# Kernel tuning notes

Measured on AMD Instinct MI355X. Metric: run time of the kernel, lower is better.

The kernel has to match this reference:

```python
import jax, jax.numpy as jnp
import numpy as np

N, E, IN = 100000, 1600000, 128
H, C = 4, 16            # heads, out_channels
HID = H * C             # concat output dim = 64
SLOPE = 0.2             # GATv2Conv negative_slope default
EPS = 1e-5              # LayerNorm eps


def setup_inputs() -> dict:
    key = jax.random.key(0)
    ks = jax.random.split(key, 12)
    s = 0.05
    x = jax.random.normal(ks[0], (N, IN), jnp.float32)
    edge_index = jax.random.randint(ks[1], (2, E), 0, N, dtype=jnp.int32)
    return {
        "x": x,
        "edge_index": edge_index,
        # GATv2Conv params (lin_l: source, lin_r: target; both with bias)
        "W_l": jax.random.normal(ks[2], (IN, HID), jnp.float32) * s,
        "b_l": jnp.zeros((HID,), jnp.float32),
        "W_r": jax.random.normal(ks[3], (IN, HID), jnp.float32) * s,
        "b_r": jnp.zeros((HID,), jnp.float32),
        "att": jax.random.normal(ks[4], (H, C), jnp.float32) * s,
        "bias": jnp.zeros((HID,), jnp.float32),
        # residual projection Linear(in, heads*out, bias=False)
        "W_res": jax.random.normal(ks[5], (IN, HID), jnp.float32) * s,
        # pyg LayerNorm affine params
        "ln_w": jnp.ones((HID,), jnp.float32),
        "ln_b": jnp.zeros((HID,), jnp.float32),
    }


def reference(x, edge_index, W_l, b_l, W_r, b_r, att, bias, W_res, ln_w, ln_b):
    n = x.shape[0]
    # GATv2Conv adds self-loops by default
    loops = jnp.arange(n, dtype=edge_index.dtype)
    src = jnp.concatenate([edge_index[0], loops])  # message source j
    dst = jnp.concatenate([edge_index[1], loops])  # message target i

    xl = (x @ W_l + b_l).reshape(n, H, C)  # source-side projection
    xr = (x @ W_r + b_r).reshape(n, H, C)  # target-side projection

    # GATv2 attention: e_ij = att . LeakyReLU(xl_j + xr_i)
    e = jax.nn.leaky_relu(xl[src] + xr[dst], SLOPE)   # [Et, H, C]
    score = jnp.einsum('ehc,hc->eh', e, att)          # [Et, H]

    # segment softmax over incoming edges of each target node
    smax = jax.ops.segment_max(score, dst, num_segments=n)
    ex = jnp.exp(score - smax[dst])
    ssum = jax.ops.segment_sum(ex, dst, num_segments=n)
    alpha = ex / (ssum[dst] + 1e-16)                  # [Et, H]

    # weighted scatter-add of source features, concat heads
    msg = xl[src] * alpha[..., None]                  # [Et, H, C]
    out = jax.ops.segment_sum(msg, dst, num_segments=n).reshape(n, HID)
    out = out + bias + x @ W_res                      # bias + residual

    # pyg.nn.LayerNorm(mode='graph', batch=None): global mean/std over all elems
    out = out - out.mean()
    out = out / (out.std() + EPS)
    return out * ln_w + ln_b
```

## Files before the change

### kernel.cpp

```cpp
#include <hip/hip_runtime.h>
#include <math.h>

#define SLOPE  0.2f
#define LN_EPS 1e-5f
#define HID    64
#define IN_DIM 128
#define BM     64

__global__ __launch_bounds__(256) void proj_kernel(
    const float* __restrict__ x,
    const float* __restrict__ Wl, const float* __restrict__ bl,
    const float* __restrict__ Wr, const float* __restrict__ br,
    const float* __restrict__ Wres,
    float* __restrict__ xl, float* __restrict__ xr, float* __restrict__ out_un,
    int n)
{
    __shared__ float xs[BM][132];
    int t = threadIdx.x;
    int row0 = blockIdx.x * BM;

#pragma unroll
    for (int p = 0; p < 8; ++p) {
        int f  = t + p * 256;
        int r  = f >> 5;
        int c4 = f & 31;
        float4 v = make_float4(0.f, 0.f, 0.f, 0.f);
        if (row0 + r < n) v = ((const float4*)x)[(long)(row0 + r) * 32 + c4];
        *(float4*)&xs[r][c4 * 4] = v;
    }
    __syncthreads();

    int cb = (t & 15) * 4;
    int ry = (t >> 4) * 4;

    float4 acc[3][4];
#pragma unroll
    for (int r = 0; r < 4; ++r) {
        acc[0][r] = *(const float4*)&bl[cb];
        acc[1][r] = *(const float4*)&br[cb];
        acc[2][r] = make_float4(0.f, 0.f, 0.f, 0.f);
    }

    for (int k4 = 0; k4 < 32; ++k4) {
        float4 xv[4];
#pragma unroll
        for (int r = 0; r < 4; ++r)
            xv[r] = *(const float4*)&xs[ry + r][k4 * 4];
#pragma unroll
        for (int kk = 0; kk < 4; ++kk) {
            int k = k4 * 4 + kk;
            float4 w0 = *(const float4*)&Wl  [k * HID + cb];
            float4 w1 = *(const float4*)&Wr  [k * HID + cb];
            float4 w2 = *(const float4*)&Wres[k * HID + cb];
#pragma unroll
            for (int r = 0; r < 4; ++r) {
                float xvk = (kk == 0) ? xv[r].x : (kk == 1) ? xv[r].y
                          : (kk == 2) ? xv[r].z : xv[r].w;
                acc[0][r].x = fmaf(xvk, w0.x, acc[0][r].x);
                acc[0][r].y = fmaf(xvk, w0.y, acc[0][r].y);
                acc[0][r].z = fmaf(xvk, w0.z, acc[0][r].z);
                acc[0][r].w = fmaf(xvk, w0.w, acc[0][r].w);
                acc[1][r].x = fmaf(xvk, w1.x, acc[1][r].x);
                acc[1][r].y = fmaf(xvk, w1.y, acc[1][r].y);
                acc[1][r].z = fmaf(xvk, w1.z, acc[1][r].z);
                acc[1][r].w = fmaf(xvk, w1.w, acc[1][r].w);
                acc[2][r].x = fmaf(xvk, w2.x, acc[2][r].x);
                acc[2][r].y = fmaf(xvk, w2.y, acc[2][r].y);
                acc[2][r].z = fmaf(xvk, w2.z, acc[2][r].z);
                acc[2][r].w = fmaf(xvk, w2.w, acc[2][r].w);
            }
        }
    }

#pragma unroll
    for (int r = 0; r < 4; ++r) {
        long ro = row0 + ry + r;
        if (ro < n) {
            *(float4*)&xl    [ro * HID + cb] = acc[0][r];
            *(float4*)&xr    [ro * HID + cb] = acc[1][r];
            *(float4*)&out_un[ro * HID + cb] = acc[2][r];
        }
    }
}

__global__ void deg_zero_kernel(int* __restrict__ deg, int n) {
    for (int i = blockIdx.x * blockDim.x + threadIdx.x; i < n; i += gridDim.x * blockDim.x)
        deg[i] = 0;
}

__global__ __launch_bounds__(256) void rank_kernel(
    const int* __restrict__ dst, int* __restrict__ deg, int* __restrict__ rank, int e)
{
    int tid = blockIdx.x * blockDim.x + threadIdx.x;
    int stride = gridDim.x * blockDim.x;
    int e4 = e >> 2;
    for (int i = tid; i < e4; i += stride) {
        int4 d = ((const int4*)dst)[i];
        int r0 = atomicAdd(&deg[d.x], 1);
        int r1 = atomicAdd(&deg[d.y], 1);
        int r2 = atomicAdd(&deg[d.z], 1);
        int r3 = atomicAdd(&deg[d.w], 1);
        ((int4*)rank)[i] = make_int4(r0, r1, r2, r3);
    }
    for (int i = (e4 << 2) + tid; i < e; i += stride)
        rank[i] = atomicAdd(&deg[dst[i]], 1);
}

__global__ __launch_bounds__(1024) void scan_kernel(
    const int* __restrict__ deg, int* __restrict__ off, int n)
{
    __shared__ int wsum[16];
    __shared__ int carry_s;
    int t = threadIdx.x, lane = t & 63, w = t >> 6;
    if (t == 0) carry_s = 0;
    __syncthreads();
    for (int base = 0; base < n; base += 4096) {
        int i0 = base + t * 4;
        int4 v = make_int4(0, 0, 0, 0);
        if (i0 + 3 < n) {
            int4 dv = *(const int4*)&deg[i0];
            v = make_int4(dv.x + 1, dv.y + 1, dv.z + 1, dv.w + 1);
        } else if (i0 < n) {
            v.x = deg[i0] + 1;
            if (i0 + 1 < n) v.y = deg[i0 + 1] + 1;
            if (i0 + 2 < n) v.z = deg[i0 + 2] + 1;
        }
        int local = v.x + v.y + v.z + v.w;
        int inc = local;
#pragma unroll
        for (int d = 1; d < 64; d <<= 1) {
            int o = __shfl_up(inc, d, 64);
            if (lane >= d) inc += o;
        }
        if (lane == 63) wsum[w] = inc;
        __syncthreads();
        if (w == 0 && lane < 16) {
            int s = wsum[lane];
#pragma unroll
            for (int d = 1; d < 16; d <<= 1) {
                int o = __shfl_up(s, d, 16);
                if (lane >= d) s += o;
            }
            wsum[lane] = s;
        }
        __syncthreads();
        int woff = (w > 0) ? wsum[w - 1] : 0;
        int bc = carry_s;
        __syncthreads();
        int o0 = bc + woff + inc - local;
        int o1 = o0 + v.x, o2 = o1 + v.y, o3 = o2 + v.z;
        if (i0     < n) off[i0]     = o0;
        if (i0 + 1 < n) off[i0 + 1] = o1;
        if (i0 + 2 < n) off[i0 + 2] = o2;
        if (i0 + 3 < n) off[i0 + 3] = o3;
        if (t == 1023) carry_s = bc + wsum[15];
        __syncthreads();
    }
    if (threadIdx.x == 0) off[n] = carry_s;
}

__global__ __launch_bounds__(256) void place_kernel(
    const int* __restrict__ src, const int* __restrict__ dst,
    const int* __restrict__ rank, const int* __restrict__ off,
    int* __restrict__ csr, int e)
{
    int tid = blockIdx.x * blockDim.x + threadIdx.x;
    int stride = gridDim.x * blockDim.x;
    int e4 = e >> 2;
    for (int i = tid; i < e4; i += stride) {
        int4 d = ((const int4*)dst)[i];
        int4 s = ((const int4*)src)[i];
        int4 r = ((const int4*)rank)[i];
        int o0 = off[d.x], o1 = off[d.y], o2 = off[d.z], o3 = off[d.w];
        csr[o0 + r.x] = s.x;
        csr[o1 + r.y] = s.y;
        csr[o2 + r.z] = s.z;
        csr[o3 + r.w] = s.w;
    }
    for (int i = (e4 << 2) + tid; i < e; i += stride)
        csr[off[dst[i]] + rank[i]] = src[i];
}

__global__ void selfloop_kernel(const int* __restrict__ off, const int* __restrict__ deg,
                                int* __restrict__ csr, int n)
{
    for (int i = blockIdx.x * blockDim.x + threadIdx.x; i < n; i += gridDim.x * blockDim.x)
        csr[off[i] + deg[i]] = i;
}

__global__ __launch_bounds__(256) void attn_kernel(
    const float* __restrict__ xl, const float* __restrict__ xr,
    const float* __restrict__ att, const float* __restrict__ bias,
    const int* __restrict__ off, const int* __restrict__ csr,
    float* __restrict__ out_un,
    float2* __restrict__ partials, int n)
{
    int lane = threadIdx.x & 63;
    int wid  = threadIdx.x >> 6;
    int node = blockIdx.x * 4 + wid;

    float s1 = 0.0f, s2 = 0.0f;
    if (node < n) {
        float a    = att[lane];
        float bi   = bias[lane];
        float xr_v = xr[(long)node * HID + lane];

        int e0 = off[node], e1 = off[node + 1];

        float m = -INFINITY, ssum = 0.0f, acc = 0.0f;

#define ATT_UPDATE(vv)                                                    \
        {                                                                 \
            float tt = (vv) + xr_v;                                       \
            tt = (tt > 0.0f) ? tt : SLOPE * tt;                           \
            float pp = tt * a;                                            \
            pp += __shfl_xor(pp, 1, 16);                                  \
            pp += __shfl_xor(pp, 2, 16);                                  \
            pp += __shfl_xor(pp, 4, 16);                                  \
            pp += __shfl_xor(pp, 8, 16);                                  \
            float nm = fmaxf(m, pp);                                      \
            float eo = __expf(m - nm);                                    \
            float pe = __expf(pp - nm);                                   \
            acc  = acc * eo + pe * (vv);                                  \
            ssum = ssum * eo + pe;                                        \
            m = nm;                                                       \
        }

        int e = e0;
        for (; e + 4 <= e1; e += 4) {
            int j0 = csr[e], j1 = csr[e + 1], j2 = csr[e + 2], j3 = csr[e + 3];
            float v0 = xl[(long)j0 * HID + lane];
            float v1 = xl[(long)j1 * HID + lane];
            float v2 = xl[(long)j2 * HID + lane];
            float v3 = xl[(long)j3 * HID + lane];
            ATT_UPDATE(v0); ATT_UPDATE(v1); ATT_UPDATE(v2); ATT_UPDATE(v3);
        }
        for (; e < e1; ++e) {
            int j = csr[e];
            float v = xl[(long)j * HID + lane];
            ATT_UPDATE(v);
        }
#undef ATT_UPDATE

        float r = acc / (ssum + 1e-16f) + bi + out_un[(long)node * HID + lane];
        out_un[(long)node * HID + lane] = r;
        s1 = r; s2 = r * r;
    }

#pragma unroll
    for (int d = 32; d; d >>= 1) {
        s1 += __shfl_xor(s1, d, 64);
        s2 += __shfl_xor(s2, d, 64);
    }
    __shared__ float bs[8];
    if (lane == 0) { bs[wid] = s1; bs[4 + wid] = s2; }
    __syncthreads();
    if (threadIdx.x == 0)
        partials[blockIdx.x] = make_float2(bs[0] + bs[1] + bs[2] + bs[3],
                                           bs[4] + bs[5] + bs[6] + bs[7]);
}

__global__ __launch_bounds__(1024) void reduce_kernel(
    const float2* __restrict__ partials, double* __restrict__ red, int nb)
{
    double a = 0.0, b = 0.0;
    for (int i = threadIdx.x; i < nb; i += 1024) {
        float2 p = partials[i];
        a += (double)p.x; b += (double)p.y;
    }
#pragma unroll
    for (int d = 32; d; d >>= 1) {
        a += __shfl_xor(a, d, 64);
        b += __shfl_xor(b, d, 64);
    }
    __shared__ double sa[16], sb[16];
    int w = threadIdx.x >> 6;
    if ((threadIdx.x & 63) == 0) { sa[w] = a; sb[w] = b; }
    __syncthreads();
    if (threadIdx.x == 0) {
        double ta = 0.0, tb = 0.0;
#pragma unroll
        for (int k = 0; k < 16; ++k) { ta += sa[k]; tb += sb[k]; }
        red[0] = ta; red[1] = tb;
    }
}

__global__ void ln_kernel(const float* __restrict__ out_un, const double* __restrict__ red,
                          const float* __restrict__ ln_w, const float* __restrict__ ln_b,
                          float* __restrict__ out, int total )
{
    double cnt  = (double)total;
    double mu   = red[0] / cnt;
    double var  = red[1] / cnt - mu * mu;
    float mean  = (float)mu;
    float inv   = 1.0f / (sqrtf((float)(var > 0.0 ? var : 0.0)) + LN_EPS);
    int n4 = total >> 2;
    for (int i = blockIdx.x * blockDim.x + threadIdx.x; i < n4; i += gridDim.x * blockDim.x) {
        float4 v = ((const float4*)out_un)[i];
        int cb = (i << 2) & 63;
        float4 r;
        r.x = (v.x - mean) * inv * ln_w[cb + 0] + ln_b[cb + 0];
        r.y = (v.y - mean) * inv * ln_w[cb + 1] + ln_b[cb + 1];
        r.z = (v.z - mean) * inv * ln_w[cb + 2] + ln_b[cb + 2];
        r.w = (v.w - mean) * inv * ln_w[cb + 3] + ln_b[cb + 3];
        ((float4*)out)[i] = r;
    }
}

extern "C" void kernel_launch(void* const* d_in, const int* in_sizes, int n_in,
                              void* d_out, int out_size, void* d_ws, size_t ws_size,
                              hipStream_t stream)
{
    const float* x    = (const float*)d_in[0];
    const int*   ei   = (const int*)d_in[1];
    const float* Wl   = (const float*)d_in[2];
    const float* bl   = (const float*)d_in[3];
    const float* Wr   = (const float*)d_in[4];
    const float* br   = (const float*)d_in[5];
    const float* att  = (const float*)d_in[6];
    const float* bias = (const float*)d_in[7];
    const float* Wres = (const float*)d_in[8];
    const float* lnw  = (const float*)d_in[9];
    const float* lnb  = (const float*)d_in[10];

    int n = in_sizes[0] / IN_DIM;
    int e = in_sizes[1] / 2;
    const int* src = ei;
    const int* dst = ei + e;

    int nblocks = (n + 3) / 4;

    char* w = (char*)d_ws;
    double* red    = (double*)w;
    float* xl      = (float*)(w + 256);
    float* xr      = xl + (long)n * HID;
    float* out_un  = xr + (long)n * HID;
    int*   deg     = (int*)(out_un + (long)n * HID);
    int*   off     = deg + n;
    int*   csr     = off + n + 1;
    int*    rank     = (int*)out_un;
    float2* partials = (float2*)deg;

    deg_zero_kernel<<<512, 256, 0, stream>>>(deg, n);
    rank_kernel<<<1024, 256, 0, stream>>>(dst, deg, rank, e);
    scan_kernel<<<1, 1024, 0, stream>>>(deg, off, n);
    place_kernel<<<1024, 256, 0, stream>>>(src, dst, rank, off, csr, e);
    selfloop_kernel<<<512, 256, 0, stream>>>(off, deg, csr, n);

    proj_kernel<<<(n + BM - 1) / BM, 256, 0, stream>>>(x, Wl, bl, Wr, br, Wres,
                                                       xl, xr, out_un, n);

    attn_kernel<<<nblocks, 256, 0, stream>>>(xl, xr, att, bias, off, csr,
                                             out_un, partials, n);
    reduce_kernel<<<1, 1024, 0, stream>>>(partials, red, nblocks);

    ln_kernel<<<4096, 256, 0, stream>>>(out_un, red, lnw, lnb, (float*)d_out, n * HID);
}
```

Before: 462.8 us.

## Process four edges per wavefront with float4 lanes and fold self-loops into scan

The attention kernel now splits each wavefront into four 16-lane groups. Each group handles a different edge using float4 loads, so four edges are processed per iteration, and the online-softmax states are merged across groups at the end with shuffles. This is meant to raise memory-level parallelism in the gather and cut the shuffle reductions per edge. The self-loop kernel is removed, with the scan writing self-loop entries directly, and the rank and place grids are doubled. The cost is extra exp and merge work plus masked lanes on low-degree nodes.

```diff
diff --git a/kernel.cpp b/kernel.cpp
--- a/kernel.cpp
+++ b/kernel.cpp
@@ -107,7 +107,7 @@
 }
 
 __global__ __launch_bounds__(1024) void scan_kernel(
-    const int* __restrict__ deg, int* __restrict__ off, int n)
+    const int* __restrict__ deg, int* __restrict__ off, int* __restrict__ csr, int n)
 {
     __shared__ int wsum[16];
     __shared__ int carry_s;
@@ -148,11 +148,11 @@
         int bc = carry_s;
         __syncthreads();
         int o0 = bc + woff + inc - local;
-        int o1 = o0 + v.x, o2 = o1 + v.y, o3 = o2 + v.z;
-        if (i0     < n) off[i0]     = o0;
-        if (i0 + 1 < n) off[i0 + 1] = o1;
-        if (i0 + 2 < n) off[i0 + 2] = o2;
-        if (i0 + 3 < n) off[i0 + 3] = o3;
+        int o1 = o0 + v.x, o2 = o1 + v.y, o3 = o2 + v.z, o4 = o3 + v.w;
+        if (i0     < n) { off[i0]     = o0; csr[o1 - 1] = i0;     }
+        if (i0 + 1 < n) { off[i0 + 1] = o1; csr[o2 - 1] = i0 + 1; }
+        if (i0 + 2 < n) { off[i0 + 2] = o2; csr[o3 - 1] = i0 + 2; }
+        if (i0 + 3 < n) { off[i0 + 3] = o3; csr[o4 - 1] = i0 + 3; }
         if (t == 1023) carry_s = bc + wsum[15];
         __syncthreads();
     }
@@ -181,13 +181,6 @@
         csr[off[dst[i]] + rank[i]] = src[i];
 }
 
-__global__ void selfloop_kernel(const int* __restrict__ off, const int* __restrict__ deg,
-                                int* __restrict__ csr, int n)
-{
-    for (int i = blockIdx.x * blockDim.x + threadIdx.x; i < n; i += gridDim.x * blockDim.x)
-        csr[off[i] + deg[i]] = i;
-}
-
 __global__ __launch_bounds__(256) void attn_kernel(
     const float* __restrict__ xl, const float* __restrict__ xr,
     const float* __restrict__ att, const float* __restrict__ bias,
@@ -195,56 +188,79 @@
     float* __restrict__ out_un,
     float2* __restrict__ partials, int n)
 {
-    int lane = threadIdx.x & 63;
-    int wid  = threadIdx.x >> 6;
-    int node = blockIdx.x * 4 + wid;
+    const int l    = threadIdx.x & 63;
+    const int wid  = threadIdx.x >> 6;
+    const int g    = l >> 4;
+    const int r    = l & 15;
+    const int node = blockIdx.x * 4 + wid;
 
     float s1 = 0.0f, s2 = 0.0f;
     if (node < n) {
-        float a    = att[lane];
-        float bi   = bias[lane];
-        float xr_v = xr[(long)node * HID + lane];
+        const float4 a4  = ((const float4*)att)[r];
+        const float4 xr4 = ((const float4*)xr)[node * 16 + r];
 
         int e0 = off[node], e1 = off[node + 1];
-
-        float m = -INFINITY, ssum = 0.0f, acc = 0.0f;
-
-#define ATT_UPDATE(vv)                                                    \
-        {                                                                 \
-            float tt = (vv) + xr_v;                                       \
-            tt = (tt > 0.0f) ? tt : SLOPE * tt;                           \
-            float pp = tt * a;                                            \
-            pp += __shfl_xor(pp, 1, 16);                                  \
-            pp += __shfl_xor(pp, 2, 16);                                  \
-            pp += __shfl_xor(pp, 4, 16);                                  \
-            pp += __shfl_xor(pp, 8, 16);                                  \
-            float nm = fmaxf(m, pp);                                      \
-            float eo = __expf(m - nm);                                    \
-            float pe = __expf(pp - nm);                                   \
-            acc  = acc * eo + pe * (vv);                                  \
-            ssum = ssum * eo + pe;                                        \
-            m = nm;                                                       \
-        }
-
-        int e = e0;
-        for (; e + 4 <= e1; e += 4) {
-            int j0 = csr[e], j1 = csr[e + 1], j2 = csr[e + 2], j3 = csr[e + 3];
-            float v0 = xl[(long)j0 * HID + lane];
-            float v1 = xl[(long)j1 * HID + lane];
-            float v2 = xl[(long)j2 * HID + lane];
-            float v3 = xl[(long)j3 * HID + lane];
-            ATT_UPDATE(v0); ATT_UPDATE(v1); ATT_UPDATE(v2); ATT_UPDATE(v3);
-        }
-        for (; e < e1; ++e) {
-            int j = csr[e];
-            float v = xl[(long)j * HID + lane];
-            ATT_UPDATE(v);
-        }
-#undef ATT_UPDATE
-
-        float r = acc / (ssum + 1e-16f) + bi + out_un[(long)node * HID + lane];
-        out_un[(long)node * HID + lane] = r;
-        s1 = r; s2 = r * r;
+        int nit = (e1 - e0 + 3) >> 2;
+
+        float m = -1e30f, ssum = 0.0f;
+        float4 acc = make_float4(0.f, 0.f, 0.f, 0.f);
+
+        for (int it = 0; it < nit; ++it) {
+            int eidx = e0 + it * 4 + g;
+            bool valid = eidx < e1;
+            int j = csr[valid ? eidx : e1 - 1];
+            float4 v = ((const float4*)xl)[j * 16 + r];
+            float tx = v.x + xr4.x, ty = v.y + xr4.y;
+            float tz = v.z + xr4.z, tw = v.w + xr4.w;
+            tx = fmaxf(tx, SLOPE * tx); ty = fmaxf(ty, SLOPE * ty);
+            tz = fmaxf(tz, SLOPE * tz); tw = fmaxf(tw, SLOPE * tw);
+            float p = fmaf(tw, a4.w, fmaf(tz, a4.z, fmaf(ty, a4.y, tx * a4.x)));
+            p += __shfl_xor(p, 1);
+            p += __shfl_xor(p, 2);
+            float s  = valid ? p : -INFINITY;
+            float nm = fmaxf(m, s);
+            float eo = __expf(m - nm);
+            float pe = __expf(s - nm);
+            acc.x = acc.x * eo + pe * v.x;
+            acc.y = acc.y * eo + pe * v.y;
+            acc.z = acc.z * eo + pe * v.z;
+            acc.w = acc.w * eo + pe * v.w;
+            ssum  = ssum * eo + pe;
+            m = nm;
+        }
+
+#pragma unroll
+        for (int mask = 16; mask <= 32; mask <<= 1) {
+            float om = __shfl_xor(m, mask);
+            float os = __shfl_xor(ssum, mask);
+            float ox = __shfl_xor(acc.x, mask);
+            float oy = __shfl_xor(acc.y, mask);
+            float oz = __shfl_xor(acc.z, mask);
+            float ow = __shfl_xor(acc.w, mask);
+            float nm = fmaxf(m, om);
+            float f1 = __expf(m - nm);
+            float f2 = __expf(om - nm);
+            acc.x = acc.x * f1 + ox * f2;
+            acc.y = acc.y * f1 + oy * f2;
+            acc.z = acc.z * f1 + oz * f2;
+            acc.w = acc.w * f1 + ow * f2;
+            ssum  = ssum * f1 + os * f2;
+            m = nm;
+        }
+
+        float inv = 1.0f / (ssum + 1e-16f);
+        if (l < 16) {
+            float4 b4  = ((const float4*)bias)[r];
+            float4 res = ((const float4*)out_un)[node * 16 + r];
+            float4 ro;
+            ro.x = acc.x * inv + b4.x + res.x;
+            ro.y = acc.y * inv + b4.y + res.y;
+            ro.z = acc.z * inv + b4.z + res.z;
+            ro.w = acc.w * inv + b4.w + res.w;
+            ((float4*)out_un)[node * 16 + r] = ro;
+            s1 = ro.x + ro.y + ro.z + ro.w;
+            s2 = ro.x * ro.x + ro.y * ro.y + ro.z * ro.z + ro.w * ro.w;
+        }
     }
 
 #pragma unroll
@@ -253,7 +269,7 @@
         s2 += __shfl_xor(s2, d, 64);
     }
     __shared__ float bs[8];
-    if (lane == 0) { bs[wid] = s1; bs[4 + wid] = s2; }
+    if (l == 0) { bs[wid] = s1; bs[4 + wid] = s2; }
     __syncthreads();
     if (threadIdx.x == 0)
         partials[blockIdx.x] = make_float2(bs[0] + bs[1] + bs[2] + bs[3],
@@ -342,10 +358,9 @@
     float2* partials = (float2*)deg;
 
     deg_zero_kernel<<<512, 256, 0, stream>>>(deg, n);
-    rank_kernel<<<1024, 256, 0, stream>>>(dst, deg, rank, e);
-    scan_kernel<<<1, 1024, 0, stream>>>(deg, off, n);
-    place_kernel<<<1024, 256, 0, stream>>>(src, dst, rank, off, csr, e);
-    selfloop_kernel<<<512, 256, 0, stream>>>(off, deg, csr, n);
+    rank_kernel<<<2048, 256, 0, stream>>>(dst, deg, rank, e);
+    scan_kernel<<<1, 1024, 0, stream>>>(deg, off, csr, n);
+    place_kernel<<<2048, 256, 0, stream>>>(src, dst, rank, off, csr, e);
 
     proj_kernel<<<(n + BM - 1) / BM, 256, 0, stream>>>(x, Wl, bl, Wr, br, Wres,
                                                        xl, xr, out_un, n);
```

After: 478.1 us. +3.3%, slower.
